# Performance work log

Hardware: AMD Instinct MI355X
Metric: run time of the kernel (lower is better)

## Reference

```python
import jax, jax.numpy as jnp
import numpy as np

DIM = 1024
N_HEADS = 16
SCALE = (DIM // N_HEADS) ** (-0.5)


def setup_inputs() -> dict:
    key = jax.random.key(0)
    kq, kk, kv = jax.random.split(key, 3)
    shape = (4, 16, 2048, 64)  # [B, H, N, Dh]
    q = jax.random.normal(kq, shape, dtype=jnp.float32)
    k = jax.random.normal(kk, shape, dtype=jnp.float32)
    v = jax.random.normal(kv, shape, dtype=jnp.float32)
    return {"q": q, "k": k, "v": v}


def reference(q, k, v):
    # Faithful translation of the torch module, INCLUDING its einsum output
    # subscripts: the second einsum is 'bhnm,bhmd->bhmd' (sums over n, keeps m),
    # exactly as written in the source.
    scores = jnp.einsum('bhnd,bhmd->bhnm', q, k) * SCALE  # [B,H,N,M]
    scores = jax.nn.softmax(scores, axis=-1)
    out = jnp.einsum('bhnm,bhmd->bhmd', scores, v)  # [B,H,M,Dh]
    return out
```

## Files before the change

kernel.cpp:

```cpp
#include <hip/hip_runtime.h>
#include <cstdint>
#include <cstddef>

#define B_    4
#define H_    16
#define N_    2048
#define D_    64
#define BH_   (B_*H_)
#define SCALE 0.125f
#define QSCL  0.18033688011f

#define P_    256
#define T_    128
#define NT    (N_/T_)
#define NP    (N_/P_)
#define TILEB 16384
#define BHB   (NT*TILEB)

typedef __attribute__((ext_vector_type(8))) short bf16x8;
typedef __attribute__((ext_vector_type(4))) float f32x4;

#if __has_builtin(__builtin_amdgcn_exp2f)
#define EXP2(x) __builtin_amdgcn_exp2f(x)
#else
#define EXP2(x) exp2f(x)
#endif

#define BARRIER() do { asm volatile("" ::: "memory"); \
                       __builtin_amdgcn_s_barrier();  \
                       asm volatile("" ::: "memory"); } while (0)

__device__ __forceinline__ short f2bf(float f) {
    union { float f; unsigned u; } x; x.f = f;
    unsigned r = x.u + 0x7FFF + ((x.u >> 16) & 1);
    return (short)(r >> 16);
}

__device__ __forceinline__ size_t swz(int row, int cc) {
    return ((size_t)(row >> 7) * TILEB) + ((row & 127) << 7) + ((cc ^ (row & 7)) << 4);
}

__device__ __forceinline__ void gload_lds16(const char* g, char* l) {
    __builtin_amdgcn_global_load_lds(
        (const __attribute__((address_space(1))) void*)g,
        (__attribute__((address_space(3))) void*)l, 16, 0, 0);
}
__device__ __forceinline__ void gload_lds4(const float* g, float* l) {
    __builtin_amdgcn_global_load_lds(
        (const __attribute__((address_space(1))) void*)g,
        (__attribute__((address_space(3))) void*)l, 4, 0, 0);
}

__global__ __launch_bounds__(512)
void mha_convert(const float* __restrict__ q, const float* __restrict__ k,
                 char* __restrict__ qk)
{
    const int gid = blockIdx.x * 512 + threadIdx.x;
    const int half = BH_ * N_ * 8;
    const bool isq = gid < half;
    const float* src = isq ? q : k;
    const float scl = isq ? QSCL : 1.0f;
    char* dst = qk + (isq ? 0 : (size_t)BH_ * BHB);
    const int id = isq ? gid : gid - half;
    const int bh  = id >> 14;
    const int row = (id >> 3) & 2047;
    const int cc  = id & 7;
    const float* p = src + ((size_t)bh * N_ + row) * D_ + cc * 8;
    float4 a = *(const float4*)p;
    float4 b = *(const float4*)(p + 4);
    bf16x8 o;
    o[0] = f2bf(a.x * scl); o[1] = f2bf(a.y * scl);
    o[2] = f2bf(a.z * scl); o[3] = f2bf(a.w * scl);
    o[4] = f2bf(b.x * scl); o[5] = f2bf(b.y * scl);
    o[6] = f2bf(b.z * scl); o[7] = f2bf(b.w * scl);
    *(bf16x8*)(dst + (size_t)bh * BHB + swz(row, cc)) = o;
}

__global__ __launch_bounds__(512)
void mha_rowsum6(const char* __restrict__ qk, float* __restrict__ rinv)
{
    __shared__ __align__(16) char KT[2][TILEB];

    const int t = threadIdx.x, w = t >> 6, l = t & 63;
    const int wid = (blockIdx.x & 7) * 64 + (blockIdx.x >> 3);
    const int bh = wid / NP, rb = wid % NP;

    const char* Qp = qk + (size_t)bh * BHB;
    const char* Kp = qk + (size_t)BH_ * BHB + (size_t)bh * BHB;

    bf16x8 af[2][2];
    #pragma unroll
    for (int rg = 0; rg < 2; ++rg)
        #pragma unroll
        for (int kh = 0; kh < 2; ++kh)
            af[rg][kh] = *(const bf16x8*)(Qp + swz(rb * P_ + w * 32 + rg * 16 + (l & 15),
                                                   kh * 4 + (l >> 4)));
    #pragma unroll
    for (int rg = 0; rg < 2; ++rg)
        #pragma unroll
        for (int kh = 0; kh < 2; ++kh)
            asm volatile("" :: "v"(af[rg][kh]));

    const int lb0 = (l & 15) * 128 + (((l >> 4) ^ (l & 7)) << 4);
    const int lb1 = (l & 15) * 128 + (((4 + (l >> 4)) ^ (l & 7)) << 4);
    const int t16 = t * 16;

    float rs[2][4] = {};

    auto STAGE = [&](int ct, int buf) {
        const char* src = Kp + (size_t)ct * TILEB;
        gload_lds16(src + t16,        KT[buf] + t16);
        gload_lds16(src + 8192 + t16, KT[buf] + 8192 + t16);
    };
    auto COMPUTE = [&](const char* kt) {
        #pragma unroll
        for (int cj = 0; cj < 8; ++cj) {
            bf16x8 b0 = *(const bf16x8*)(kt + lb0 + cj * 2048);
            bf16x8 b1 = *(const bf16x8*)(kt + lb1 + cj * 2048);
            #pragma unroll
            for (int rg = 0; rg < 2; ++rg) {
                f32x4 c = {0.f, 0.f, 0.f, 0.f};
                c = __builtin_amdgcn_mfma_f32_16x16x32_bf16(af[rg][0], b0, c, 0, 0, 0);
                c = __builtin_amdgcn_mfma_f32_16x16x32_bf16(af[rg][1], b1, c, 0, 0, 0);
                rs[rg][0] += EXP2(c[0]);
                rs[rg][1] += EXP2(c[1]);
                rs[rg][2] += EXP2(c[2]);
                rs[rg][3] += EXP2(c[3]);
            }
        }
    };

    STAGE(0, 0);
    STAGE(1, 1);
    #pragma unroll 1
    for (int ct = 0; ct < NT - 2; ++ct) {
        asm volatile("s_waitcnt vmcnt(2)" ::: "memory");
        BARRIER();
        COMPUTE(KT[ct & 1]);
        BARRIER();
        STAGE(ct + 2, ct & 1);
    }
    asm volatile("s_waitcnt vmcnt(2)" ::: "memory");
    BARRIER();
    COMPUTE(KT[(NT - 2) & 1]);
    asm volatile("s_waitcnt vmcnt(0)" ::: "memory");
    BARRIER();
    COMPUTE(KT[(NT - 1) & 1]);

    #pragma unroll
    for (int rg = 0; rg < 2; ++rg)
        #pragma unroll
        for (int i = 0; i < 4; ++i) {
            rs[rg][i] += __shfl_xor(rs[rg][i], 1);
            rs[rg][i] += __shfl_xor(rs[rg][i], 2);
            rs[rg][i] += __shfl_xor(rs[rg][i], 4);
            rs[rg][i] += __shfl_xor(rs[rg][i], 8);
        }
    if ((l & 15) == 0) {
        #pragma unroll
        for (int rg = 0; rg < 2; ++rg) {
            const int rbase = rb * P_ + w * 32 + rg * 16 + (l >> 4) * 4;
            #pragma unroll
            for (int i = 0; i < 4; ++i)
                rinv[(size_t)bh * N_ + rbase + i] = 1.0f / rs[rg][i];
        }
    }
}

__global__ __launch_bounds__(512)
void mha_colsum6(const char* __restrict__ qk, const float* __restrict__ rinv,
                 const float* __restrict__ v, float* __restrict__ out)
{
    __shared__ __align__(16) char QT[2][TILEB];
    __shared__ float rvw[2][8][T_];
    __shared__ float cs[P_];

    const int t = threadIdx.x, w = t >> 6, l = t & 63;
    const int wid = (blockIdx.x & 7) * 64 + (blockIdx.x >> 3);
    const int bh = wid / NP, cb = wid % NP;

    const char* Qp = qk + (size_t)bh * BHB;
    const char* Kp = qk + (size_t)BH_ * BHB + (size_t)bh * BHB;
    const float* Rg = rinv + (size_t)bh * N_;

    bf16x8 kf[2][2];
    #pragma unroll
    for (int rg = 0; rg < 2; ++rg)
        #pragma unroll
        for (int kh = 0; kh < 2; ++kh)
            kf[rg][kh] = *(const bf16x8*)(Kp + swz(cb * P_ + w * 32 + rg * 16 + (l & 15),
                                                    kh * 4 + (l >> 4)));
    #pragma unroll
    for (int rg = 0; rg < 2; ++rg)
        #pragma unroll
        for (int kh = 0; kh < 2; ++kh)
            asm volatile("" :: "v"(kf[rg][kh]));

    const int lb0 = (l & 15) * 128 + (((l >> 4) ^ (l & 7)) << 4);
    const int lb1 = (l & 15) * 128 + (((4 + (l >> 4)) ^ (l & 7)) << 4);
    const int t16 = t * 16;

    float ca[2] = {0.f, 0.f};

    auto STAGE = [&](int rt, int buf) {
        const char* src = Qp + (size_t)rt * TILEB;
        gload_lds16(src + t16,        QT[buf] + t16);
        gload_lds16(src + 8192 + t16, QT[buf] + 8192 + t16);
        const float* rsrc = Rg + rt * T_;
        float* rdst = &rvw[buf][w][0];
        gload_lds4(rsrc + l,      rdst + l);
        gload_lds4(rsrc + 64 + l, rdst + 64 + l);
    };
    auto COMPUTE = [&](const char* qt, const float* rvb) {
        #pragma unroll
        for (int rj = 0; rj < 8; ++rj) {
            bf16x8 a0 = *(const bf16x8*)(qt + lb0 + rj * 2048);
            bf16x8 a1 = *(const bf16x8*)(qt + lb1 + rj * 2048);
            float4 r4 = *(const float4*)(rvb + rj * 16 + (l >> 4) * 4);
            #pragma unroll
            for (int rg = 0; rg < 2; ++rg) {
                f32x4 c = {0.f, 0.f, 0.f, 0.f};
                c = __builtin_amdgcn_mfma_f32_16x16x32_bf16(a0, kf[rg][0], c, 0, 0, 0);
                c = __builtin_amdgcn_mfma_f32_16x16x32_bf16(a1, kf[rg][1], c, 0, 0, 0);
                ca[rg] += EXP2(c[0]) * r4.x + EXP2(c[1]) * r4.y
                        + EXP2(c[2]) * r4.z + EXP2(c[3]) * r4.w;
            }
        }
    };

    STAGE(0, 0);
    STAGE(1, 1);
    #pragma unroll 1
    for (int rt = 0; rt < NT - 2; ++rt) {
        asm volatile("s_waitcnt vmcnt(4)" ::: "memory");
        BARRIER();
        COMPUTE(QT[rt & 1], &rvw[rt & 1][w][0]);
        BARRIER();
        STAGE(rt + 2, rt & 1);
    }
    asm volatile("s_waitcnt vmcnt(4)" ::: "memory");
    BARRIER();
    COMPUTE(QT[(NT - 2) & 1], &rvw[(NT - 2) & 1][w][0]);
    asm volatile("s_waitcnt vmcnt(0)" ::: "memory");
    BARRIER();
    COMPUTE(QT[(NT - 1) & 1], &rvw[(NT - 1) & 1][w][0]);

    #pragma unroll
    for (int rg = 0; rg < 2; ++rg) {
        ca[rg] += __shfl_xor(ca[rg], 16);
        ca[rg] += __shfl_xor(ca[rg], 32);
    }
    if (l < 16) { cs[w * 32 + l] = ca[0]; cs[w * 32 + 16 + l] = ca[1]; }
    __syncthreads();

    const float4* Vg = (const float4*)(v + ((size_t)bh * N_ + cb * P_) * D_);
    float4* Og = (float4*)(out + ((size_t)bh * N_ + cb * P_) * D_);
    #pragma unroll
    for (int i = 0; i < 8; ++i) {
        int id = i * 512 + t;
        float s = cs[id >> 4];
        float4 vv = Vg[id];
        float4 o; o.x = vv.x * s; o.y = vv.y * s; o.z = vv.z * s; o.w = vv.w * s;
        Og[id] = o;
    }
}

#define FTS 128
#define FNT 16

__device__ __forceinline__ bf16x8 cvt8(const float* p) {
    float4 a = *(const float4*)p;
    float4 b = *(const float4*)(p + 4);
    bf16x8 r;
    r[0] = f2bf(a.x); r[1] = f2bf(a.y); r[2] = f2bf(a.z); r[3] = f2bf(a.w);
    r[4] = f2bf(b.x); r[5] = f2bf(b.y); r[6] = f2bf(b.z); r[7] = f2bf(b.w);
    return r;
}
__device__ __forceinline__ void fstage(char* lds, const float* src, int t) {
    #pragma unroll
    for (int i = 0; i < 2; ++i) {
        int ch = i * 512 + t, r = ch >> 3, cc = ch & 7;
        bf16x8 v = cvt8(src + (size_t)r * D_ + cc * 8);
        *(bf16x8*)(lds + r * 128 + ((cc ^ (r & 7)) << 4)) = v;
    }
}
__device__ __forceinline__ bf16x8 fread(const char* lds, int row, int cc) {
    return *(const bf16x8*)(lds + row * 128 + ((cc ^ (row & 7)) << 4));
}

__global__ __launch_bounds__(512)
void mha_rowsum_fb(const float* __restrict__ q, const float* __restrict__ k,
                   float* __restrict__ rinv)
{
    __shared__ __align__(16) char KT[FTS * 128];
    const int t = threadIdx.x, w = t >> 6, l = t & 63;
    const int bh = blockIdx.x / FNT, rb = blockIdx.x % FNT;
    const float* Qg = q + (size_t)bh * N_ * D_;
    const float* Kg = k + (size_t)bh * N_ * D_;
    const int qrow = rb * FTS + w * 16 + (l & 15);
    bf16x8 af[2];
    #pragma unroll
    for (int kh = 0; kh < 2; ++kh)
        af[kh] = cvt8(Qg + (size_t)qrow * D_ + kh * 32 + (l >> 4) * 8);
    float rs[4] = {0.f, 0.f, 0.f, 0.f};
    for (int ct = 0; ct < FNT; ++ct) {
        __syncthreads();
        fstage(KT, Kg + (size_t)ct * FTS * D_, t);
        __syncthreads();
        #pragma unroll
        for (int cj = 0; cj < 8; ++cj) {
            const int krow = cj * 16 + (l & 15);
            f32x4 c = {0.f, 0.f, 0.f, 0.f};
            #pragma unroll
            for (int kh = 0; kh < 2; ++kh)
                c = __builtin_amdgcn_mfma_f32_16x16x32_bf16(af[kh], fread(KT, krow, kh * 4 + (l >> 4)), c, 0, 0, 0);
            rs[0] += __expf(c[0] * SCALE); rs[1] += __expf(c[1] * SCALE);
            rs[2] += __expf(c[2] * SCALE); rs[3] += __expf(c[3] * SCALE);
        }
    }
    #pragma unroll
    for (int i = 0; i < 4; ++i) {
        rs[i] += __shfl_xor(rs[i], 1); rs[i] += __shfl_xor(rs[i], 2);
        rs[i] += __shfl_xor(rs[i], 4); rs[i] += __shfl_xor(rs[i], 8);
    }
    if ((l & 15) == 0) {
        const int rbase = rb * FTS + w * 16 + (l >> 4) * 4;
        #pragma unroll
        for (int i = 0; i < 4; ++i)
            rinv[(size_t)bh * N_ + rbase + i] = 1.0f / rs[i];
    }
}

__global__ __launch_bounds__(512)
void mha_colsum_fb(const float* __restrict__ q, const float* __restrict__ k,
                   const float* __restrict__ v, const float* __restrict__ rinv,
                   float* __restrict__ out)
{
    __shared__ __align__(16) char QT[FTS * 128];
    __shared__ float rv[FTS];
    __shared__ float cs[FTS];
    const int t = threadIdx.x, w = t >> 6, l = t & 63;
    const int bh = blockIdx.x / FNT, cb = blockIdx.x % FNT;
    const float* Qg = q + (size_t)bh * N_ * D_;
    const float* Kg = k + (size_t)bh * N_ * D_;
    const float* Rg = rinv + (size_t)bh * N_;
    const int kcol = cb * FTS + w * 16 + (l & 15);
    bf16x8 kf[2];
    #pragma unroll
    for (int kh = 0; kh < 2; ++kh)
        kf[kh] = cvt8(Kg + (size_t)kcol * D_ + kh * 32 + (l >> 4) * 8);
    float ca = 0.f;
    for (int rt = 0; rt < FNT; ++rt) {
        __syncthreads();
        fstage(QT, Qg + (size_t)rt * FTS * D_, t);
        if (t < FTS) rv[t] = Rg[rt * FTS + t];
        __syncthreads();
        #pragma unroll
        for (int rj = 0; rj < 8; ++rj) {
            const int qr = rj * 16 + (l & 15);
            f32x4 c = {0.f, 0.f, 0.f, 0.f};
            #pragma unroll
            for (int kh = 0; kh < 2; ++kh)
                c = __builtin_amdgcn_mfma_f32_16x16x32_bf16(fread(QT, qr, kh * 4 + (l >> 4)), kf[kh], c, 0, 0, 0);
            float4 r4 = *(const float4*)&rv[rj * 16 + (l >> 4) * 4];
            ca += __expf(c[0] * SCALE) * r4.x + __expf(c[1] * SCALE) * r4.y
                + __expf(c[2] * SCALE) * r4.z + __expf(c[3] * SCALE) * r4.w;
        }
    }
    ca += __shfl_xor(ca, 16); ca += __shfl_xor(ca, 32);
    if (l < 16) cs[w * 16 + l] = ca;
    __syncthreads();
    const float4* Vg = (const float4*)(v + (size_t)bh * N_ * D_ + (size_t)cb * FTS * D_);
    float4* Og = (float4*)(out + (size_t)bh * N_ * D_ + (size_t)cb * FTS * D_);
    #pragma unroll
    for (int i = 0; i < 4; ++i) {
        int id = i * 512 + t;
        float s = cs[id >> 4];
        float4 vv = Vg[id];
        float4 o; o.x = vv.x * s; o.y = vv.y * s; o.z = vv.z * s; o.w = vv.w * s;
        Og[id] = o;
    }
}

extern "C" void kernel_launch(void* const* d_in, const int* in_sizes, int n_in,
                              void* d_out, int out_size, void* d_ws, size_t ws_size,
                              hipStream_t stream)
{
    const float* q = (const float*)d_in[0];
    const float* k = (const float*)d_in[1];
    const float* v = (const float*)d_in[2];
    float* out = (float*)d_out;

    const size_t qkBytes = (size_t)2 * BH_ * BHB;
    const size_t need = qkBytes + (size_t)BH_ * N_ * 4;

    if (ws_size >= need) {
        char* qk = (char*)d_ws;
        float* rinv = (float*)(qk + qkBytes);
        mha_convert<<<dim3(2 * BH_ * N_ * 8 / 512), dim3(512), 0, stream>>>(q, k, qk);
        mha_rowsum6<<<dim3(BH_ * NP), dim3(512), 0, stream>>>(qk, rinv);
        mha_colsum6<<<dim3(BH_ * NP), dim3(512), 0, stream>>>(qk, rinv, v, out);
    } else {
        float* rinv = (float*)d_ws;
        mha_rowsum_fb<<<dim3(BH_ * FNT), dim3(512), 0, stream>>>(q, k, rinv);
        mha_colsum_fb<<<dim3(BH_ * FNT), dim3(512), 0, stream>>>(q, k, v, rinv, out);
    }
}
```

Measured before the change: 108.6 us.

## Split row/column sum kernels across the reduction dimension with atomic partials

The row-sum and column-sum kernels now use 256-thread blocks over 128-row tiles, and each tile's reduction dimension is split into two halves handled by separate blocks. That gives 2048 blocks per kernel instead of 512. Partial sums are merged with global atomicAdd, and a per-tile ticket counter lets the last finishing block compute the reciprocal or scale V into the output. The convert kernel now also zeroes the accumulators and counters. The aim is better occupancy and load balance across CUs, at the cost of atomic traffic, extra workspace, and order-dependent float summation.

```diff
diff --git a/kernel.cpp b/kernel.cpp
--- a/kernel.cpp
+++ b/kernel.cpp
@@ -10,12 +10,12 @@
 #define SCALE 0.125f
 #define QSCL  0.18033688011f
 
-#define P_    256
-#define T_    128
-#define NT    (N_/T_)
-#define NP    (N_/P_)
+#define NTC   16
+#define TB64  8192
 #define TILEB 16384
-#define BHB   (NT*TILEB)
+#define BHB   (16*TILEB)
+#define QKB   ((size_t)2*BH_*BHB)
+#define NZW   (BH_*N_)
 
 typedef __attribute__((ext_vector_type(8))) short bf16x8;
 typedef __attribute__((ext_vector_type(4))) float f32x4;
@@ -56,6 +56,8 @@
                  char* __restrict__ qk)
 {
     const int gid = blockIdx.x * 512 + threadIdx.x;
+    if (gid < 2 * NZW + 4096)
+        ((int*)(qk + QKB))[gid] = 0;
     const int half = BH_ * N_ * 8;
     const bool isq = gid < half;
     const float* src = isq ? q : k;
@@ -76,24 +78,26 @@
     *(bf16x8*)(dst + (size_t)bh * BHB + swz(row, cc)) = o;
 }
 
-__global__ __launch_bounds__(512)
-void mha_rowsum6(const char* __restrict__ qk, float* __restrict__ rinv)
-{
-    __shared__ __align__(16) char KT[2][TILEB];
+__global__ __launch_bounds__(256, 6)
+void mha_rowsum7(const char* __restrict__ qk, float* __restrict__ Z,
+                 float* __restrict__ RI, int* __restrict__ TK)
+{
+    __shared__ __align__(16) char KT[2][TB64];
+    __shared__ int go;
 
     const int t = threadIdx.x, w = t >> 6, l = t & 63;
-    const int wid = (blockIdx.x & 7) * 64 + (blockIdx.x >> 3);
-    const int bh = wid / NP, rb = wid % NP;
+    const int wid = (blockIdx.x & 7) * 256 + (blockIdx.x >> 3);
+    const int bh = wid >> 5, r = wid & 31, rb = r & 15, mc = r >> 4;
 
     const char* Qp = qk + (size_t)bh * BHB;
-    const char* Kp = qk + (size_t)BH_ * BHB + (size_t)bh * BHB;
+    const char* Kc = qk + (size_t)BH_ * BHB + (size_t)bh * BHB + (size_t)mc * NTC * TB64;
 
     bf16x8 af[2][2];
     #pragma unroll
     for (int rg = 0; rg < 2; ++rg)
         #pragma unroll
         for (int kh = 0; kh < 2; ++kh)
-            af[rg][kh] = *(const bf16x8*)(Qp + swz(rb * P_ + w * 32 + rg * 16 + (l & 15),
+            af[rg][kh] = *(const bf16x8*)(Qp + swz(rb * 128 + w * 32 + rg * 16 + (l & 15),
                                                    kh * 4 + (l >> 4)));
     #pragma unroll
     for (int rg = 0; rg < 2; ++rg)
@@ -108,13 +112,13 @@
     float rs[2][4] = {};
 
     auto STAGE = [&](int ct, int buf) {
-        const char* src = Kp + (size_t)ct * TILEB;
+        const char* src = Kc + (size_t)ct * TB64;
         gload_lds16(src + t16,        KT[buf] + t16);
-        gload_lds16(src + 8192 + t16, KT[buf] + 8192 + t16);
+        gload_lds16(src + 4096 + t16, KT[buf] + 4096 + t16);
     };
     auto COMPUTE = [&](const char* kt) {
         #pragma unroll
-        for (int cj = 0; cj < 8; ++cj) {
+        for (int cj = 0; cj < 4; ++cj) {
             bf16x8 b0 = *(const bf16x8*)(kt + lb0 + cj * 2048);
             bf16x8 b1 = *(const bf16x8*)(kt + lb1 + cj * 2048);
             #pragma unroll
@@ -133,7 +137,7 @@
     STAGE(0, 0);
     STAGE(1, 1);
     #pragma unroll 1
-    for (int ct = 0; ct < NT - 2; ++ct) {
+    for (int ct = 0; ct < NTC - 2; ++ct) {
         asm volatile("s_waitcnt vmcnt(2)" ::: "memory");
         BARRIER();
         COMPUTE(KT[ct & 1]);
@@ -142,10 +146,10 @@
     }
     asm volatile("s_waitcnt vmcnt(2)" ::: "memory");
     BARRIER();
-    COMPUTE(KT[(NT - 2) & 1]);
+    COMPUTE(KT[(NTC - 2) & 1]);
     asm volatile("s_waitcnt vmcnt(0)" ::: "memory");
     BARRIER();
-    COMPUTE(KT[(NT - 1) & 1]);
+    COMPUTE(KT[(NTC - 1) & 1]);
 
     #pragma unroll
     for (int rg = 0; rg < 2; ++rg)
@@ -159,36 +163,49 @@
     if ((l & 15) == 0) {
         #pragma unroll
         for (int rg = 0; rg < 2; ++rg) {
-            const int rbase = rb * P_ + w * 32 + rg * 16 + (l >> 4) * 4;
+            const int rbase = bh * N_ + rb * 128 + w * 32 + rg * 16 + (l >> 4) * 4;
             #pragma unroll
             for (int i = 0; i < 4; ++i)
-                rinv[(size_t)bh * N_ + rbase + i] = 1.0f / rs[rg][i];
-        }
-    }
-}
-
-__global__ __launch_bounds__(512)
-void mha_colsum6(const char* __restrict__ qk, const float* __restrict__ rinv,
+                atomicAdd(&Z[rbase + i], rs[rg][i]);
+        }
+    }
+    __syncthreads();
+    if (t == 0) go = (atomicAdd(&TK[bh * 16 + rb], 1) == 1);
+    __syncthreads();
+    if (go) {
+        __threadfence();
+        if (t < 128) {
+            const int idx = bh * N_ + rb * 128 + t;
+            float z = __hip_atomic_load(&Z[idx], __ATOMIC_RELAXED, __HIP_MEMORY_SCOPE_AGENT);
+            RI[idx] = 1.0f / z;
+        }
+    }
+}
+
+__global__ __launch_bounds__(256, 6)
+void mha_colsum7(const char* __restrict__ qk, const float* __restrict__ RI,
+                 float* __restrict__ CS, int* __restrict__ TK,
                  const float* __restrict__ v, float* __restrict__ out)
 {
-    __shared__ __align__(16) char QT[2][TILEB];
-    __shared__ float rvw[2][8][T_];
-    __shared__ float cs[P_];
+    __shared__ __align__(16) char QT[2][TB64];
+    __shared__ float rvw[2][4][64];
+    __shared__ float lcs[128];
+    __shared__ int go;
 
     const int t = threadIdx.x, w = t >> 6, l = t & 63;
-    const int wid = (blockIdx.x & 7) * 64 + (blockIdx.x >> 3);
-    const int bh = wid / NP, cb = wid % NP;
-
-    const char* Qp = qk + (size_t)bh * BHB;
+    const int wid = (blockIdx.x & 7) * 256 + (blockIdx.x >> 3);
+    const int bh = wid >> 5, r = wid & 31, cb = r & 15, nc = r >> 4;
+
+    const char* Qc = qk + (size_t)bh * BHB + (size_t)nc * NTC * TB64;
     const char* Kp = qk + (size_t)BH_ * BHB + (size_t)bh * BHB;
-    const float* Rg = rinv + (size_t)bh * N_;
+    const float* Rc = RI + (size_t)bh * N_ + nc * (NTC * 64);
 
     bf16x8 kf[2][2];
     #pragma unroll
     for (int rg = 0; rg < 2; ++rg)
         #pragma unroll
         for (int kh = 0; kh < 2; ++kh)
-            kf[rg][kh] = *(const bf16x8*)(Kp + swz(cb * P_ + w * 32 + rg * 16 + (l & 15),
+            kf[rg][kh] = *(const bf16x8*)(Kp + swz(cb * 128 + w * 32 + rg * 16 + (l & 15),
                                                     kh * 4 + (l >> 4)));
     #pragma unroll
     for (int rg = 0; rg < 2; ++rg)
@@ -203,20 +220,17 @@
     float ca[2] = {0.f, 0.f};
 
     auto STAGE = [&](int rt, int buf) {
-        const char* src = Qp + (size_t)rt * TILEB;
+        const char* src = Qc + (size_t)rt * TB64;
         gload_lds16(src + t16,        QT[buf] + t16);
-        gload_lds16(src + 8192 + t16, QT[buf] + 8192 + t16);
-        const float* rsrc = Rg + rt * T_;
-        float* rdst = &rvw[buf][w][0];
-        gload_lds4(rsrc + l,      rdst + l);
-        gload_lds4(rsrc + 64 + l, rdst + 64 + l);
+        gload_lds16(src + 4096 + t16, QT[buf] + 4096 + t16);
+        gload_lds4(Rc + rt * 64 + l, &rvw[buf][w][0] + l);
     };
     auto COMPUTE = [&](const char* qt, const float* rvb) {
         #pragma unroll
-        for (int rj = 0; rj < 8; ++rj) {
-            bf16x8 a0 = *(const bf16x8*)(qt + lb0 + rj * 2048);
-            bf16x8 a1 = *(const bf16x8*)(qt + lb1 + rj * 2048);
-            float4 r4 = *(const float4*)(rvb + rj * 16 + (l >> 4) * 4);
+        for (int cj = 0; cj < 4; ++cj) {
+            bf16x8 a0 = *(const bf16x8*)(qt + lb0 + cj * 2048);
+            bf16x8 a1 = *(const bf16x8*)(qt + lb1 + cj * 2048);
+            float4 r4 = *(const float4*)(rvb + cj * 16 + (l >> 4) * 4);
             #pragma unroll
             for (int rg = 0; rg < 2; ++rg) {
                 f32x4 c = {0.f, 0.f, 0.f, 0.f};
@@ -231,37 +245,48 @@
     STAGE(0, 0);
     STAGE(1, 1);
     #pragma unroll 1
-    for (int rt = 0; rt < NT - 2; ++rt) {
-        asm volatile("s_waitcnt vmcnt(4)" ::: "memory");
+    for (int rt = 0; rt < NTC - 2; ++rt) {
+        asm volatile("s_waitcnt vmcnt(3)" ::: "memory");
         BARRIER();
         COMPUTE(QT[rt & 1], &rvw[rt & 1][w][0]);
         BARRIER();
         STAGE(rt + 2, rt & 1);
     }
-    asm volatile("s_waitcnt vmcnt(4)" ::: "memory");
+    asm volatile("s_waitcnt vmcnt(3)" ::: "memory");
     BARRIER();
-    COMPUTE(QT[(NT - 2) & 1], &rvw[(NT - 2) & 1][w][0]);
+    COMPUTE(QT[(NTC - 2) & 1], &rvw[(NTC - 2) & 1][w][0]);
     asm volatile("s_waitcnt vmcnt(0)" ::: "memory");
     BARRIER();
-    COMPUTE(QT[(NT - 1) & 1], &rvw[(NT - 1) & 1][w][0]);
+    COMPUTE(QT[(NTC - 1) & 1], &rvw[(NTC - 1) & 1][w][0]);
 
     #pragma unroll
     for (int rg = 0; rg < 2; ++rg) {
         ca[rg] += __shfl_xor(ca[rg], 16);
         ca[rg] += __shfl_xor(ca[rg], 32);
     }
-    if (l < 16) { cs[w * 32 + l] = ca[0]; cs[w * 32 + 16 + l] = ca[1]; }
+    if (l < 16) {
+        atomicAdd(&CS[bh * N_ + cb * 128 + w * 32 + l],      ca[0]);
+        atomicAdd(&CS[bh * N_ + cb * 128 + w * 32 + 16 + l], ca[1]);
+    }
     __syncthreads();
-
-    const float4* Vg = (const float4*)(v + ((size_t)bh * N_ + cb * P_) * D_);
-    float4* Og = (float4*)(out + ((size_t)bh * N_ + cb * P_) * D_);
-    #pragma unroll
-    for (int i = 0; i < 8; ++i) {
-        int id = i * 512 + t;
-        float s = cs[id >> 4];
-        float4 vv = Vg[id];
-        float4 o; o.x = vv.x * s; o.y = vv.y * s; o.z = vv.z * s; o.w = vv.w * s;
-        Og[id] = o;
+    if (t == 0) go = (atomicAdd(&TK[1024 + bh * 16 + cb], 1) == 1);
+    __syncthreads();
+    if (go) {
+        __threadfence();
+        if (t < 128)
+            lcs[t] = __hip_atomic_load(&CS[bh * N_ + cb * 128 + t],
+                                       __ATOMIC_RELAXED, __HIP_MEMORY_SCOPE_AGENT);
+        __syncthreads();
+        const float4* Vg = (const float4*)(v + ((size_t)bh * N_ + cb * 128) * D_);
+        float4* Og = (float4*)(out + ((size_t)bh * N_ + cb * 128) * D_);
+        #pragma unroll
+        for (int i = 0; i < 8; ++i) {
+            int id = i * 256 + t;
+            float s = lcs[id >> 4];
+            float4 vv = Vg[id];
+            float4 o; o.x = vv.x * s; o.y = vv.y * s; o.z = vv.z * s; o.w = vv.w * s;
+            Og[id] = o;
+        }
     }
 }
 
@@ -391,15 +416,17 @@
     const float* v = (const float*)d_in[2];
     float* out = (float*)d_out;
 
-    const size_t qkBytes = (size_t)2 * BH_ * BHB;
-    const size_t need = qkBytes + (size_t)BH_ * N_ * 4;
+    const size_t need = QKB + (size_t)NZW * 4 * 3 + 16384;
 
     if (ws_size >= need) {
-        char* qk = (char*)d_ws;
-        float* rinv = (float*)(qk + qkBytes);
+        char*  qk = (char*)d_ws;
+        float* Z  = (float*)(qk + QKB);
+        float* CS = Z + NZW;
+        int*   TK = (int*)(CS + NZW);
+        float* RI = (float*)((char*)TK + 16384);
         mha_convert<<<dim3(2 * BH_ * N_ * 8 / 512), dim3(512), 0, stream>>>(q, k, qk);
-        mha_rowsum6<<<dim3(BH_ * NP), dim3(512), 0, stream>>>(qk, rinv);
-        mha_colsum6<<<dim3(BH_ * NP), dim3(512), 0, stream>>>(qk, rinv, v, out);
+        mha_rowsum7<<<dim3(2048), dim3(256), 0, stream>>>(qk, Z, RI, TK);
+        mha_colsum7<<<dim3(2048), dim3(256), 0, stream>>>(qk, RI, CS, TK, v, out);
     } else {
         float* rinv = (float*)d_ws;
         mha_rowsum_fb<<<dim3(BH_ * FNT), dim3(512), 0, stream>>>(q, k, rinv);
```

Result: slower. 280.2 us (+158.1%).
